# Kernel optimization log

Measured on AMD Instinct MI355X. Metric: run time of the kernel, lower is better.

## Reference

```python
import jax, jax.numpy as jnp
import numpy as np

T, B, D, H, A = 512, 1024, 128, 64, 18


def _mlp(x, W1, b1, W2, b2):
    # two Linear+ReLU layers (MLP with hidden_sizes=(64,64), output_dim=0)
    h = jax.nn.relu(x @ W1.T + b1)
    return jax.nn.relu(h @ W2.T + b2)


def _gru_scan(x, dones, h0, Wih, Whh, bih, bhh):
    # x: [T,B,H], dones: [T,B], h0: [1,B,H]; torch GRU cell with done-reset
    def step(h, inp):
        xt, dt = inp
        h = (1.0 - dt)[:, None] * h  # reset state where episode ended
        gi = xt @ Wih.T + bih        # [B,3H]
        gh = h @ Whh.T + bhh
        ir, iz, i_n = jnp.split(gi, 3, axis=-1)
        hr, hz, h_n = jnp.split(gh, 3, axis=-1)
        r = jax.nn.sigmoid(ir + hr)
        z = jax.nn.sigmoid(iz + hz)
        n = jnp.tanh(i_n + r * h_n)
        h_new = (1.0 - z) * n + z * h
        return h_new, h_new
    hT, hs = jax.lax.scan(step, h0[0], (x, dones))
    return hs, hT[None]  # [T,B,H], [1,B,H]


def setup_inputs() -> dict:
    key = jax.random.key(0)
    ks = jax.random.split(key, 24)
    u = lambda k, shape, fan_in: jax.random.uniform(k, shape, jnp.float32, -1.0, 1.0) / np.sqrt(fan_in)
    inp = {
        'obs': jax.random.normal(ks[0], (T, B, D), jnp.float32),
        'dones': (jax.random.uniform(ks[1], (T, B)) < 0.01).astype(jnp.float32),
        'actor_state': jnp.zeros((1, B, H), jnp.float32),
        'critic_state': jnp.zeros((1, B, H), jnp.float32),
        # actor params
        'aW1': u(ks[2], (H, D), D), 'ab1': u(ks[3], (H,), D),
        'aW2': u(ks[4], (H, H), H), 'ab2': u(ks[5], (H,), H),
        'aWih': u(ks[6], (3 * H, H), H), 'aWhh': u(ks[7], (3 * H, H), H),
        'abih': u(ks[8], (3 * H,), H), 'abhh': u(ks[9], (3 * H,), H),
        'aWl': u(ks[10], (A, H), H), 'abl': u(ks[11], (A,), H),
        # critic params
        'cW1': u(ks[12], (H, D), D), 'cb1': u(ks[13], (H,), D),
        'cW2': u(ks[14], (H, H), H), 'cb2': u(ks[15], (H,), H),
        'cWih': u(ks[16], (3 * H, H), H), 'cWhh': u(ks[17], (3 * H, H), H),
        'cbih': u(ks[18], (3 * H,), H), 'cbhh': u(ks[19], (3 * H,), H),
        'cWv': u(ks[20], (1, H), H), 'cbv': u(ks[21], (1,), H),
    }
    return inp


def reference(obs, dones, actor_state, critic_state,
              aW1, ab1, aW2, ab2, aWih, aWhh, abih, abhh, aWl, abl,
              cW1, cb1, cW2, cb2, cWih, cWhh, cbih, cbhh, cWv, cbv):
    # actor branch
    xa = _mlp(obs, aW1, ab1, aW2, ab2)                              # [T,B,H]
    ha, actor_state = _gru_scan(xa, dones, actor_state, aWih, aWhh, abih, abhh)
    logits = ha @ aWl.T + abl                                       # [T,B,A]
    # critic branch
    xc = _mlp(obs, cW1, cb1, cW2, cb2)
    hc, critic_state = _gru_scan(xc, dones, critic_state, cWih, cWhh, cbih, cbhh)
    values = hc @ cWv.T + cbv                                       # [T,B,1]
    return (logits, values, actor_state, critic_state)
```

## Files before the change

### kernel.cpp

```cpp
#include <hip/hip_runtime.h>
#include <hip/hip_bf16.h>

typedef short short8 __attribute__((ext_vector_type(8)));
typedef float f32x4 __attribute__((ext_vector_type(4)));

#define T_ 512
#define B_ 1024
#define D_ 128
#define H_ 64
#define A_ 18
#define TB_ (T_*B_)

#define XELEMS (TB_*H_)
#define WBASE  (2*XELEMS)
#define WBR    38912
#define W1OFF  0
#define W2OFF  8192
#define WIHOFF 12288
#define WHHOFF 24576
#define WHDOFF 36864

#define LOGN  (TB_*A_)
#define VOFF_ LOGN
#define SOFF_ (LOGN + TB_)

#define S1_ (-1.4426950408889634f)
#define S2_ (-2.885390081777927f)

__device__ __forceinline__ ushort f2bf(float f) {
  __hip_bfloat16 h = __float2bfloat16(f);
  return __builtin_bit_cast(ushort, h);
}
__device__ __forceinline__ uint cvt_pk_bf16(float lo, float hi) {
  uint r;
  asm("v_cvt_pk_bf16_f32 %0, %1, %2" : "=v"(r) : "v"(lo), "v"(hi));
  return r;
}
__device__ __forceinline__ ushort cvt1_bf16(float v) {
  return (ushort)(cvt_pk_bf16(v, v) & 0xffffu);
}
__device__ __forceinline__ f32x4 mfma16(short8 a, short8 b, f32x4 c) {
  return __builtin_amdgcn_mfma_f32_16x16x32_bf16(a, b, c, 0, 0, 0);
}

__global__ __launch_bounds__(256) void prep_kernel(
    const float* aW1, const float* aW2, const float* aWih, const float* aWhh, const float* aWl,
    const float* cW1, const float* cW2, const float* cWih, const float* cWhh, const float* cWv,
    ushort* wts) {
  int idx = blockIdx.x * 256 + threadIdx.x;
  if (idx >= 2*WBR) return;
  int br = idx / WBR, off = idx % WBR;
  float v;
  if      (off < W2OFF)  v = (br ? cW1  : aW1 )[off];
  else if (off < WIHOFF) v = (br ? cW2  : aW2 )[off - W2OFF];
  else if (off < WHHOFF) {
    int rel = off - WIHOFF;
    v = (br ? cWih : aWih)[rel];
    v *= (rel < 128*H_) ? S1_ : S2_;
  }
  else if (off < WHDOFF) {
    int rel = off - WHHOFF;
    v = (br ? cWhh : aWhh)[rel];
    v *= (rel < 128*H_) ? S1_ : S2_;
  }
  else {
    int t = off - WHDOFF;
    if (br == 0) v = (t < A_*H_) ? aWl[t] : 0.f;
    else         v = (t < H_)    ? cWv[t] : 0.f;
  }
  wts[WBASE + idx] = f2bf(v);
}

__global__ __launch_bounds__(256) void mlp_kernel(
    const float* __restrict__ obs, const ushort* __restrict__ wts,
    const float* __restrict__ ab1, const float* __restrict__ ab2,
    const float* __restrict__ cb1, const float* __restrict__ cb2,
    ushort* __restrict__ xout) {
  __shared__ __align__(16) ushort htA[4][16 * H_], htC[4][16 * H_];
  __shared__ __align__(16) ushort wlds[24576];
  const int tid = threadIdx.x;
  const int l = tid & 63, w = tid >> 6;
  const int lr = l & 15, lg = l >> 4;
  const int key = lr & 7;
  const long base = (long)blockIdx.x * 256;
  const ushort* wbA = wts + WBASE;
  const ushort* wbC = wts + WBASE + WBR;

  const int colq[2] = {lr, 16 + lr};
  float b1A[4], b1C[4], b2A[4], b2C[4];
  #pragma unroll
  for (int nt = 0; nt < 4; ++nt) {
    int coln = nt * 16 + lr;
    b1A[nt] = ab1[coln]; b1C[nt] = cb1[coln];
    b2A[nt] = ab2[coln]; b2C[nt] = cb2[coln];
  }
  (void)colq;

  #pragma unroll
  for (int i = 0; i < 12; ++i) {
    int c = tid + i * 256;
    int seg = (c < 1024) ? 0 : (c < 2048) ? 1 : (c < 2560) ? 2 : 3;
    int cbase = (seg == 0) ? 0 : (seg == 1) ? 1024 : (seg == 2) ? 2048 : 2560;
    int off = (c - cbase) * 8;
    int L = (seg < 2) ? 128 : 64;
    int segdst = (seg == 0) ? 0 : (seg == 1) ? 8192 : (seg == 2) ? 16384 : 20480;
    const ushort* src = (seg == 0) ? wbA + W1OFF + off :
                        (seg == 1) ? wbC + W1OFF + off :
                        (seg == 2) ? wbA + W2OFF + off : wbC + W2OFF + off;
    int n = off / L, ci = (off % L) / 8;
    int cis = (ci & ~7) | ((ci & 7) ^ (n & 7));
    *(uint4*)(wlds + segdst + n * L + cis * 8) = *(const uint4*)src;
  }
  __syncthreads();

  auto getW1 = [&](int br, int n, int ks) -> short8 {
    int ci = ks * 4 + lg;
    int cis = (ci & 8) | ((ci & 7) ^ (n & 7));
    return *(const short8*)(wlds + br * 8192 + n * D_ + cis * 8);
  };
  auto getW2 = [&](int br, int n, int ks) -> short8 {
    int ci = ks * 4 + lg;
    int cis = ci ^ (n & 7);
    return *(const short8*)(wlds + 16384 + br * 4096 + n * H_ + cis * 8);
  };

  auto ldobs = [&](int s, float4 (&buf)[8]) {
    const float* op = obs + (base + s * 64 + (long)w * 16 + lr) * D_;
    #pragma unroll
    for (int ks = 0; ks < 4; ++ks) {
      buf[2 * ks]     = *(const float4*)(op + ks * 32 + lg * 8);
      buf[2 * ks + 1] = *(const float4*)(op + ks * 32 + lg * 8 + 4);
    }
  };

  auto compute = [&](int s, float4 (&buf)[8]) {
    short8 af[4];
    #pragma unroll
    for (int ks = 0; ks < 4; ++ks) {
      uint4 u;
      u.x = cvt_pk_bf16(buf[2 * ks].x, buf[2 * ks].y);
      u.y = cvt_pk_bf16(buf[2 * ks].z, buf[2 * ks].w);
      u.z = cvt_pk_bf16(buf[2 * ks + 1].x, buf[2 * ks + 1].y);
      u.w = cvt_pk_bf16(buf[2 * ks + 1].z, buf[2 * ks + 1].w);
      af[ks] = __builtin_bit_cast(short8, u);
    }
    f32x4 aA[4], aC[4];
    #pragma unroll
    for (int nt = 0; nt < 4; ++nt) {
      aA[nt] = f32x4{b1A[nt], b1A[nt], b1A[nt], b1A[nt]};
      aC[nt] = f32x4{b1C[nt], b1C[nt], b1C[nt], b1C[nt]};
    }
    #pragma unroll
    for (int ks = 0; ks < 4; ++ks) {
      #pragma unroll
      for (int nt = 0; nt < 4; ++nt) {
        int n = nt * 16 + lr;
        aA[nt] = mfma16(af[ks], getW1(0, n, ks), aA[nt]);
        aC[nt] = mfma16(af[ks], getW1(1, n, ks), aC[nt]);
      }
    }
    #pragma unroll
    for (int nt = 0; nt < 4; ++nt) {
      int coln = nt * 16 + lr;
      #pragma unroll
      for (int j = 0; j < 4; ++j) {
        int rw = lg * 4 + j;
        int idx = rw * H_ + ((((coln >> 3) ^ (rw & 7))) << 3) + (coln & 7);
        htA[w][idx] = cvt1_bf16(fmaxf(aA[nt][j], 0.f));
        htC[w][idx] = cvt1_bf16(fmaxf(aC[nt][j], 0.f));
      }
    }
    short8 a2A[2], a2C[2];
    #pragma unroll
    for (int ks = 0; ks < 2; ++ks) {
      int c = ks * 4 + lg;
      a2A[ks] = *(const short8*)(&htA[w][lr * H_ + ((c ^ key) << 3)]);
      a2C[ks] = *(const short8*)(&htC[w][lr * H_ + ((c ^ key) << 3)]);
    }
    f32x4 cA[4], cC[4];
    #pragma unroll
    for (int nt = 0; nt < 4; ++nt) {
      cA[nt] = f32x4{b2A[nt], b2A[nt], b2A[nt], b2A[nt]};
      cC[nt] = f32x4{b2C[nt], b2C[nt], b2C[nt], b2C[nt]};
    }
    #pragma unroll
    for (int ks = 0; ks < 2; ++ks) {
      #pragma unroll
      for (int nt = 0; nt < 4; ++nt) {
        int n = nt * 16 + lr;
        cA[nt] = mfma16(a2A[ks], getW2(0, n, ks), cA[nt]);
        cC[nt] = mfma16(a2C[ks], getW2(1, n, ks), cC[nt]);
      }
    }
    #pragma unroll
    for (int nt = 0; nt < 4; ++nt) {
      int coln = nt * 16 + lr;
      #pragma unroll
      for (int j = 0; j < 4; ++j) {
        int rw = lg * 4 + j;
        int idx = rw * H_ + ((((coln >> 3) ^ (rw & 7))) << 3) + (coln & 7);
        htA[w][idx] = cvt1_bf16(fmaxf(cA[nt][j], 0.f));
        htC[w][idx] = cvt1_bf16(fmaxf(cC[nt][j], 0.f));
      }
    }
    {
      long rt = base + s * 64 + (long)w * 16;
      ushort* dpA = xout + (size_t)rt * H_;
      ushort* dpC = xout + (size_t)XELEMS + (size_t)rt * H_;
      #pragma unroll
      for (int i = 0; i < 2; ++i) {
        int id = l + i * 64;
        int rr = id >> 3, cc = id & 7;
        uint4 vA = *(const uint4*)(&htA[w][rr * H_ + ((cc ^ (rr & 7)) << 3)]);
        *(uint4*)(dpA + rr * H_ + (cc << 3)) = vA;
        uint4 vC = *(const uint4*)(&htC[w][rr * H_ + ((cc ^ (rr & 7)) << 3)]);
        *(uint4*)(dpC + rr * H_ + (cc << 3)) = vC;
      }
    }
  };

  float4 bufA[8], bufB[8];
  ldobs(0, bufA);
  ldobs(1, bufB);
  compute(0, bufA);
  ldobs(2, bufA);
  compute(1, bufB);
  ldobs(3, bufB);
  compute(2, bufA);
  compute(3, bufB);
}

__global__ __launch_bounds__(256, 1) void scan_kernel(
    const ushort* __restrict__ wts,
    const ushort* __restrict__ xin,
    ushort* __restrict__ hist,
    const float* __restrict__ dones,
    const float* __restrict__ astate, const float* __restrict__ cstate,
    const float* __restrict__ abih, const float* __restrict__ abhh,
    const float* __restrict__ cbih, const float* __restrict__ cbhh,
    float* __restrict__ out) {
  __shared__ __align__(16) ushort hbuf[2][16 * H_];
  __shared__ __align__(8)  ushort dl16[T_ * 16];
  const int tid = threadIdx.x;
  const int l = tid & 63, w = tid >> 6;
  const int lr = l & 15, lg = l >> 4;
  const int grp = blockIdx.x & 1;
  const int b0 = (blockIdx.x >> 1) * 16;

  const ushort* wb = wts + grp * WBR;
  const ushort* xp = xin + (size_t)grp * XELEMS;
  ushort* hp = hist + (size_t)grp * XELEMS;
  const float* bihp = grp ? cbih : abih;
  const float* bhhp = grp ? cbhh : abhh;
  const float* st   = grp ? cstate : astate;

  #pragma unroll
  for (int i = 0; i < 8; ++i) {
    int s = tid + i * 256;
    int t = s >> 2, p = s & 3;
    float4 v = *(const float4*)(dones + (size_t)t * B_ + b0 + p * 4);
    uint lo = (v.x != 0.f ? 1u : 0u) | ((v.y != 0.f ? 1u : 0u) << 16);
    uint hi = (v.z != 0.f ? 1u : 0u) | ((v.w != 0.f ? 1u : 0u) << 16);
    *(uint2*)(&dl16[t * 16 + p * 4]) = uint2{lo, hi};
  }

  short8 ihW[3][2], hhW[3][2];
  #pragma unroll
  for (int g = 0; g < 3; ++g) {
    int n = g * 64 + w * 16 + lr;
    #pragma unroll
    for (int ks = 0; ks < 2; ++ks) {
      ihW[g][ks] = *(const short8*)(wb + WIHOFF + n * H_ + ks * 32 + lg * 8);
      hhW[g][ks] = *(const short8*)(wb + WHHOFF + n * H_ + ks * 32 + lg * 8);
    }
  }

  const int o4 = w * 16 + lg * 4;
  f32x4 bs0, bs1, binv, bhnv;
  {
    float4 a0 = *(const float4*)(bihp + o4),       h0v = *(const float4*)(bhhp + o4);
    float4 a1 = *(const float4*)(bihp + 64 + o4),  h1v = *(const float4*)(bhhp + 64 + o4);
    float4 a2 = *(const float4*)(bihp + 128 + o4), h2v = *(const float4*)(bhhp + 128 + o4);
    bs0[0]=S1_*(a0.x+h0v.x); bs0[1]=S1_*(a0.y+h0v.y); bs0[2]=S1_*(a0.z+h0v.z); bs0[3]=S1_*(a0.w+h0v.w);
    bs1[0]=S1_*(a1.x+h1v.x); bs1[1]=S1_*(a1.y+h1v.y); bs1[2]=S1_*(a1.z+h1v.z); bs1[3]=S1_*(a1.w+h1v.w);
    binv[0]=S2_*a2.x; binv[1]=S2_*a2.y; binv[2]=S2_*a2.z; binv[3]=S2_*a2.w;
    bhnv[0]=S2_*h2v.x; bhnv[1]=S2_*h2v.y; bhnv[2]=S2_*h2v.z; bhnv[3]=S2_*h2v.w;
  }

  const int myW = lr * H_ + (((w * 2 + (lg >> 1)) ^ (lr & 7)) << 3) + (lg & 1) * 4;
  const int rdA = lr * H_ + (((0 + lg) ^ (lr & 7)) << 3);
  const int rdB = lr * H_ + (((4 + lg) ^ (lr & 7)) << 3);

  float h_old[4];
  {
    float4 h0v = *(const float4*)(st + (size_t)(b0 + lr) * H_ + o4);
    bool rs0 = (dones[b0 + lr] != 0.f);
    h_old[0] = rs0 ? 0.f : h0v.x; h_old[1] = rs0 ? 0.f : h0v.y;
    h_old[2] = rs0 ? 0.f : h0v.z; h_old[3] = rs0 ? 0.f : h0v.w;
    uint2 hv;
    hv.x = cvt_pk_bf16(h_old[0], h_old[1]);
    hv.y = cvt_pk_bf16(h_old[2], h_old[3]);
    *(uint2*)(&hbuf[0][myW]) = hv;
  }

  __syncthreads();

  auto loadx = [&](int t, short8 (&f)[2]) {
    const ushort* p = xp + ((size_t)t * B_ + b0 + lr) * H_;
    f[0] = *(const short8*)(p + lg * 8);
    f[1] = *(const short8*)(p + 32 + lg * 8);
  };

  short8 buf0[2], buf1[2], buf2[2], buf3[2];
  loadx(0, buf0); loadx(1, buf1); loadx(2, buf2); loadx(3, buf3);

  f32x4 preA[3], preB[3];
  auto cpre = [&](short8 (&xb)[2], f32x4 (&pre)[3]) {
    pre[0] = bs0;  pre[1] = bs1;  pre[2] = binv;
    pre[0] = mfma16(ihW[0][0], xb[0], pre[0]); pre[0] = mfma16(ihW[0][1], xb[1], pre[0]);
    pre[1] = mfma16(ihW[1][0], xb[0], pre[1]); pre[1] = mfma16(ihW[1][1], xb[1], pre[1]);
    pre[2] = mfma16(ihW[2][0], xb[0], pre[2]); pre[2] = mfma16(ihW[2][1], xb[1], pre[2]);
  };
  cpre(buf0, preA);

  int cur = 0;

  auto dostep = [&](int t, short8 (&xcur)[2], short8 (&xnext)[2],
                    f32x4 (&preU)[3], f32x4 (&preN)[3]) {
    short8 hf0 = *(const short8*)(&hbuf[cur][rdA]);
    short8 hf1 = *(const short8*)(&hbuf[cur][rdB]);
    int tn = t + 1;
    ushort dn = dl16[((tn < T_) ? tn : 0) * 16 + lr];
    bool rs = (tn < T_) && (dn != 0);

    f32x4 S0 = preU[0], S1 = preU[1], Gh = bhnv;
    S0 = mfma16(hhW[0][0], hf0, S0); S0 = mfma16(hhW[0][1], hf1, S0);
    S1 = mfma16(hhW[1][0], hf0, S1); S1 = mfma16(hhW[1][1], hf1, S1);
    Gh = mfma16(hhW[2][0], hf0, Gh); Gh = mfma16(hhW[2][1], hf1, Gh);

    cpre(xnext, preN);
    int tp = (t + 4 < T_) ? t + 4 : T_ - 1;
    loadx(tp, xcur);

    float hn[4];
    #pragma unroll
    for (int j = 0; j < 4; ++j) {
      float rr = __builtin_amdgcn_rcpf(1.f + __builtin_amdgcn_exp2f(S0[j]));
      float zz = __builtin_amdgcn_rcpf(1.f + __builtin_amdgcn_exp2f(S1[j]));
      float sn = fmaf(rr, Gh[j], preU[2][j]);
      float qq = __builtin_amdgcn_rcpf(1.f + __builtin_amdgcn_exp2f(sn));
      float nn = fmaf(2.f, qq, -1.f);
      hn[j] = fmaf(zz, h_old[j] - nn, nn);
    }
    uint2 hv;
    hv.x = cvt_pk_bf16(hn[0], hn[1]);
    hv.y = cvt_pk_bf16(hn[2], hn[3]);
    *(uint2*)(hp + ((size_t)t * B_ + b0 + lr) * H_ + o4) = hv;
    uint2 hz;
    hz.x = rs ? 0u : hv.x;
    hz.y = rs ? 0u : hv.y;
    h_old[0] = rs ? 0.f : hn[0]; h_old[1] = rs ? 0.f : hn[1];
    h_old[2] = rs ? 0.f : hn[2]; h_old[3] = rs ? 0.f : hn[3];
    int nxt = cur ^ 1;
    *(uint2*)(&hbuf[nxt][myW]) = hz;
    asm volatile("s_waitcnt lgkmcnt(0)" ::: "memory");
    __builtin_amdgcn_s_barrier();
    cur = nxt;
  };

  for (int it = 0; it < T_ / 4; ++it) {
    dostep(4 * it,     buf0, buf1, preA, preB);
    dostep(4 * it + 1, buf1, buf2, preB, preA);
    dostep(4 * it + 2, buf2, buf3, preA, preB);
    dostep(4 * it + 3, buf3, buf0, preB, preA);
  }

  float4 fs = {h_old[0], h_old[1], h_old[2], h_old[3]};
  *(float4*)(out + SOFF_ + (size_t)grp * (B_ * H_) + (size_t)(b0 + lr) * H_ + o4) = fs;
}

__global__ __launch_bounds__(256) void head_kernel(
    const ushort* __restrict__ ws,
    const float* __restrict__ abl, const float* __restrict__ cbv,
    float* __restrict__ out) {
  __shared__ float ltile[4][16 * A_];
  const int tid = threadIdx.x;
  const int l = tid & 63, w = tid >> 6;
  const int lr = l & 15, lg = l >> 4;
  const long r0 = (long)blockIdx.x * 64 + w * 16;
  const f32x4 fzero = {0.f, 0.f, 0.f, 0.f};

  const ushort* hA = ws + r0 * H_;
  const ushort* hC = ws + XELEMS + r0 * H_;
  short8 aA[2], aC[2];
  #pragma unroll
  for (int ks = 0; ks < 2; ++ks) {
    aA[ks] = *(const short8*)(hA + lr * H_ + ks * 32 + lg * 8);
    aC[ks] = *(const short8*)(hC + lr * H_ + ks * 32 + lg * 8);
  }
  const ushort* wbA = ws + WBASE + WHDOFF;
  const ushort* wbC = ws + WBASE + WBR + WHDOFF;
  f32x4 acc[2];
  acc[0] = fzero; acc[1] = fzero;
  #pragma unroll
  for (int nt = 0; nt < 2; ++nt) {
    int n = nt * 16 + lr;
    #pragma unroll
    for (int ks = 0; ks < 2; ++ks) {
      short8 b = *(const short8*)(wbA + n * H_ + ks * 32 + lg * 8);
      acc[nt] = mfma16(aA[ks], b, acc[nt]);
    }
  }
  f32x4 vacc = fzero;
  {
    int n = lr;
    #pragma unroll
    for (int ks = 0; ks < 2; ++ks) {
      short8 b = *(const short8*)(wbC + n * H_ + ks * 32 + lg * 8);
      vacc = mfma16(aC[ks], b, vacc);
    }
  }
  #pragma unroll
  for (int nt = 0; nt < 2; ++nt) {
    int n = nt * 16 + lr;
    if (n < A_) {
      float bias = abl[n];
      #pragma unroll
      for (int j = 0; j < 4; ++j)
        ltile[w][(lg * 4 + j) * A_ + n] = acc[nt][j] + bias;
    }
  }
  asm volatile("s_waitcnt lgkmcnt(0)" ::: "memory");
  #pragma unroll
  for (int i = 0; i < 5; ++i) {
    int idx = l + i * 64;
    if (idx < 16 * A_)
      out[r0 * A_ + idx] = ltile[w][idx];
  }
  if (lr == 0) {
    float bias = cbv[0];
    #pragma unroll
    for (int j = 0; j < 4; ++j)
      out[VOFF_ + r0 + lg * 4 + j] = vacc[j] + bias;
  }
}

extern "C" void kernel_launch(void* const* d_in, const int* in_sizes, int n_in,
                              void* d_out, int out_size, void* d_ws, size_t ws_size,
                              hipStream_t stream) {
  const float* obs    = (const float*)d_in[0];
  const float* dones  = (const float*)d_in[1];
  const float* astate = (const float*)d_in[2];
  const float* cstate = (const float*)d_in[3];
  const float* aW1  = (const float*)d_in[4];
  const float* ab1  = (const float*)d_in[5];
  const float* aW2  = (const float*)d_in[6];
  const float* ab2  = (const float*)d_in[7];
  const float* aWih = (const float*)d_in[8];
  const float* aWhh = (const float*)d_in[9];
  const float* abih = (const float*)d_in[10];
  const float* abhh = (const float*)d_in[11];
  const float* aWl  = (const float*)d_in[12];
  const float* abl  = (const float*)d_in[13];
  const float* cW1  = (const float*)d_in[14];
  const float* cb1  = (const float*)d_in[15];
  const float* cW2  = (const float*)d_in[16];
  const float* cb2  = (const float*)d_in[17];
  const float* cWih = (const float*)d_in[18];
  const float* cWhh = (const float*)d_in[19];
  const float* cbih = (const float*)d_in[20];
  const float* cbhh = (const float*)d_in[21];
  const float* cWv  = (const float*)d_in[22];
  const float* cbv  = (const float*)d_in[23];
  ushort* ws = (ushort*)d_ws;
  float* out = (float*)d_out;

  const size_t need = ((size_t)2 * XELEMS + 2 * WBR) * 2;
  if (ws_size < need) {
    hipMemsetAsync(d_out, 0x7F, 16, stream);
    return;
  }

  hipLaunchKernelGGL(prep_kernel, dim3(304), dim3(256), 0, stream,
                     aW1, aW2, aWih, aWhh, aWl, cW1, cW2, cWih, cWhh, cWv, ws);
  hipLaunchKernelGGL(mlp_kernel, dim3(TB_ / 256), dim3(256), 0, stream,
                     obs, ws, ab1, ab2, cb1, cb2, ws);
  hipLaunchKernelGGL(scan_kernel, dim3(128), dim3(256), 0, stream,
                     ws + WBASE, ws, ws, dones, astate, cstate,
                     abih, abhh, cbih, cbhh, out);
  hipLaunchKernelGGL(head_kernel, dim3(TB_ / 64), dim3(256), 0, stream,
                     ws, abl, cbv, out);
}
```

Baseline: 343.0 us.

## Process actor and critic GRU scans together per block with 8-row batches

The scan kernel now has each block handle both the actor and critic GRUs for 8 batch rows, instead of one GRU for 16 rows. The grid grows from 128 to 128 blocks of 8 rows each, but every block does two independent recurrences. Their MFMA chains can interleave within a single barrier per step, hiding latency and halving the number of per-step barriers across the two scans. In exchange, half of the MFMA rows are duplicated padding (lanes 8-15 repeat rows 0-7), which wastes compute, and register pressure doubles.

Result: slower. 470.4 us (+37.1%).

```diff
diff --git a/kernel.cpp b/kernel.cpp
--- a/kernel.cpp
+++ b/kernel.cpp
@@ -86,7 +86,6 @@
   const ushort* wbA = wts + WBASE;
   const ushort* wbC = wts + WBASE + WBR;
 
-  const int colq[2] = {lr, 16 + lr};
   float b1A[4], b1C[4], b2A[4], b2C[4];
   #pragma unroll
   for (int nt = 0; nt < 4; ++nt) {
@@ -94,7 +93,6 @@
     b1A[nt] = ab1[coln]; b1C[nt] = cb1[coln];
     b2A[nt] = ab2[coln]; b2C[nt] = cb2[coln];
   }
-  (void)colq;
 
   #pragma unroll
   for (int i = 0; i < 12; ++i) {
@@ -239,144 +237,194 @@
     const float* __restrict__ abih, const float* __restrict__ abhh,
     const float* __restrict__ cbih, const float* __restrict__ cbhh,
     float* __restrict__ out) {
-  __shared__ __align__(16) ushort hbuf[2][16 * H_];
-  __shared__ __align__(8)  ushort dl16[T_ * 16];
+  __shared__ __align__(16) ushort hbufA[2][16 * H_];
+  __shared__ __align__(16) ushort hbufC[2][16 * H_];
+  __shared__ __align__(8)  ushort dl8[T_ * 8];
   const int tid = threadIdx.x;
   const int l = tid & 63, w = tid >> 6;
   const int lr = l & 15, lg = l >> 4;
-  const int grp = blockIdx.x & 1;
-  const int b0 = (blockIdx.x >> 1) * 16;
-
-  const ushort* wb = wts + grp * WBR;
-  const ushort* xp = xin + (size_t)grp * XELEMS;
-  ushort* hp = hist + (size_t)grp * XELEMS;
-  const float* bihp = grp ? cbih : abih;
-  const float* bhhp = grp ? cbhh : abhh;
-  const float* st   = grp ? cstate : astate;
-
-  #pragma unroll
-  for (int i = 0; i < 8; ++i) {
-    int s = tid + i * 256;
-    int t = s >> 2, p = s & 3;
-    float4 v = *(const float4*)(dones + (size_t)t * B_ + b0 + p * 4);
-    uint lo = (v.x != 0.f ? 1u : 0u) | ((v.y != 0.f ? 1u : 0u) << 16);
-    uint hi = (v.z != 0.f ? 1u : 0u) | ((v.w != 0.f ? 1u : 0u) << 16);
-    *(uint2*)(&dl16[t * 16 + p * 4]) = uint2{lo, hi};
-  }
-
-  short8 ihW[3][2], hhW[3][2];
+  const int lrb = lr & 7;
+  const int b0 = blockIdx.x * 8;
+
+  const ushort* wbA = wts;
+  const ushort* wbC = wts + WBR;
+  const ushort* xpA = xin;
+  const ushort* xpC = xin + (size_t)XELEMS;
+  ushort* hpA = hist;
+  ushort* hpC = hist + (size_t)XELEMS;
+
+  #pragma unroll
+  for (int i = 0; i < 16; ++i) {
+    int idx = tid + i * 256;
+    int t = idx >> 3, p = idx & 7;
+    dl8[idx] = (dones[(size_t)t * B_ + b0 + p] != 0.f) ? 1 : 0;
+    (void)t; (void)p;
+  }
+
+  short8 ihA[3][2], hhA[3][2], ihC[3][2], hhC[3][2];
   #pragma unroll
   for (int g = 0; g < 3; ++g) {
     int n = g * 64 + w * 16 + lr;
     #pragma unroll
     for (int ks = 0; ks < 2; ++ks) {
-      ihW[g][ks] = *(const short8*)(wb + WIHOFF + n * H_ + ks * 32 + lg * 8);
-      hhW[g][ks] = *(const short8*)(wb + WHHOFF + n * H_ + ks * 32 + lg * 8);
+      ihA[g][ks] = *(const short8*)(wbA + WIHOFF + n * H_ + ks * 32 + lg * 8);
+      hhA[g][ks] = *(const short8*)(wbA + WHHOFF + n * H_ + ks * 32 + lg * 8);
+      ihC[g][ks] = *(const short8*)(wbC + WIHOFF + n * H_ + ks * 32 + lg * 8);
+      hhC[g][ks] = *(const short8*)(wbC + WHHOFF + n * H_ + ks * 32 + lg * 8);
     }
   }
 
   const int o4 = w * 16 + lg * 4;
-  f32x4 bs0, bs1, binv, bhnv;
-  {
-    float4 a0 = *(const float4*)(bihp + o4),       h0v = *(const float4*)(bhhp + o4);
-    float4 a1 = *(const float4*)(bihp + 64 + o4),  h1v = *(const float4*)(bhhp + 64 + o4);
-    float4 a2 = *(const float4*)(bihp + 128 + o4), h2v = *(const float4*)(bhhp + 128 + o4);
-    bs0[0]=S1_*(a0.x+h0v.x); bs0[1]=S1_*(a0.y+h0v.y); bs0[2]=S1_*(a0.z+h0v.z); bs0[3]=S1_*(a0.w+h0v.w);
-    bs1[0]=S1_*(a1.x+h1v.x); bs1[1]=S1_*(a1.y+h1v.y); bs1[2]=S1_*(a1.z+h1v.z); bs1[3]=S1_*(a1.w+h1v.w);
-    binv[0]=S2_*a2.x; binv[1]=S2_*a2.y; binv[2]=S2_*a2.z; binv[3]=S2_*a2.w;
-    bhnv[0]=S2_*h2v.x; bhnv[1]=S2_*h2v.y; bhnv[2]=S2_*h2v.z; bhnv[3]=S2_*h2v.w;
+  f32x4 bsA0, bsA1, bnA, bhA, bsC0, bsC1, bnC, bhC;
+  #pragma unroll
+  for (int q = 0; q < 2; ++q) {
+    const float* bi = q ? cbih : abih;
+    const float* bh = q ? cbhh : abhh;
+    float4 a0 = *(const float4*)(bi + o4),       h0v = *(const float4*)(bh + o4);
+    float4 a1 = *(const float4*)(bi + 64 + o4),  h1v = *(const float4*)(bh + 64 + o4);
+    float4 a2 = *(const float4*)(bi + 128 + o4), h2v = *(const float4*)(bh + 128 + o4);
+    f32x4 s0, s1, nv, hv;
+    s0[0]=S1_*(a0.x+h0v.x); s0[1]=S1_*(a0.y+h0v.y); s0[2]=S1_*(a0.z+h0v.z); s0[3]=S1_*(a0.w+h0v.w);
+    s1[0]=S1_*(a1.x+h1v.x); s1[1]=S1_*(a1.y+h1v.y); s1[2]=S1_*(a1.z+h1v.z); s1[3]=S1_*(a1.w+h1v.w);
+    nv[0]=S2_*a2.x; nv[1]=S2_*a2.y; nv[2]=S2_*a2.z; nv[3]=S2_*a2.w;
+    hv[0]=S2_*h2v.x; hv[1]=S2_*h2v.y; hv[2]=S2_*h2v.z; hv[3]=S2_*h2v.w;
+    if (q) { bsC0=s0; bsC1=s1; bnC=nv; bhC=hv; } else { bsA0=s0; bsA1=s1; bnA=nv; bhA=hv; }
   }
 
   const int myW = lr * H_ + (((w * 2 + (lg >> 1)) ^ (lr & 7)) << 3) + (lg & 1) * 4;
   const int rdA = lr * H_ + (((0 + lg) ^ (lr & 7)) << 3);
   const int rdB = lr * H_ + (((4 + lg) ^ (lr & 7)) << 3);
 
-  float h_old[4];
+  float hA_old[4], hC_old[4];
   {
-    float4 h0v = *(const float4*)(st + (size_t)(b0 + lr) * H_ + o4);
-    bool rs0 = (dones[b0 + lr] != 0.f);
-    h_old[0] = rs0 ? 0.f : h0v.x; h_old[1] = rs0 ? 0.f : h0v.y;
-    h_old[2] = rs0 ? 0.f : h0v.z; h_old[3] = rs0 ? 0.f : h0v.w;
+    float4 ha = *(const float4*)(astate + (size_t)(b0 + lrb) * H_ + o4);
+    float4 hc = *(const float4*)(cstate + (size_t)(b0 + lrb) * H_ + o4);
+    bool rs0 = (dones[b0 + lrb] != 0.f);
+    hA_old[0] = rs0 ? 0.f : ha.x; hA_old[1] = rs0 ? 0.f : ha.y;
+    hA_old[2] = rs0 ? 0.f : ha.z; hA_old[3] = rs0 ? 0.f : ha.w;
+    hC_old[0] = rs0 ? 0.f : hc.x; hC_old[1] = rs0 ? 0.f : hc.y;
+    hC_old[2] = rs0 ? 0.f : hc.z; hC_old[3] = rs0 ? 0.f : hc.w;
     uint2 hv;
-    hv.x = cvt_pk_bf16(h_old[0], h_old[1]);
-    hv.y = cvt_pk_bf16(h_old[2], h_old[3]);
-    *(uint2*)(&hbuf[0][myW]) = hv;
+    hv.x = cvt_pk_bf16(hA_old[0], hA_old[1]);
+    hv.y = cvt_pk_bf16(hA_old[2], hA_old[3]);
+    *(uint2*)(&hbufA[0][myW]) = hv;
+    hv.x = cvt_pk_bf16(hC_old[0], hC_old[1]);
+    hv.y = cvt_pk_bf16(hC_old[2], hC_old[3]);
+    *(uint2*)(&hbufC[0][myW]) = hv;
   }
 
   __syncthreads();
 
-  auto loadx = [&](int t, short8 (&f)[2]) {
-    const ushort* p = xp + ((size_t)t * B_ + b0 + lr) * H_;
+  auto loadx = [&](const ushort* xp, int t, short8 (&f)[2]) {
+    const ushort* p = xp + ((size_t)t * B_ + b0 + lrb) * H_;
     f[0] = *(const short8*)(p + lg * 8);
     f[1] = *(const short8*)(p + 32 + lg * 8);
   };
 
-  short8 buf0[2], buf1[2], buf2[2], buf3[2];
-  loadx(0, buf0); loadx(1, buf1); loadx(2, buf2); loadx(3, buf3);
-
-  f32x4 preA[3], preB[3];
-  auto cpre = [&](short8 (&xb)[2], f32x4 (&pre)[3]) {
-    pre[0] = bs0;  pre[1] = bs1;  pre[2] = binv;
-    pre[0] = mfma16(ihW[0][0], xb[0], pre[0]); pre[0] = mfma16(ihW[0][1], xb[1], pre[0]);
-    pre[1] = mfma16(ihW[1][0], xb[0], pre[1]); pre[1] = mfma16(ihW[1][1], xb[1], pre[1]);
-    pre[2] = mfma16(ihW[2][0], xb[0], pre[2]); pre[2] = mfma16(ihW[2][1], xb[1], pre[2]);
-  };
-  cpre(buf0, preA);
+  short8 bA0[2], bA1[2], bA2[2], bA3[2], bC0[2], bC1[2], bC2[2], bC3[2];
+  loadx(xpA, 0, bA0); loadx(xpA, 1, bA1); loadx(xpA, 2, bA2); loadx(xpA, 3, bA3);
+  loadx(xpC, 0, bC0); loadx(xpC, 1, bC1); loadx(xpC, 2, bC2); loadx(xpC, 3, bC3);
+
+  f32x4 pAa[3], pAb[3], pCa[3], pCb[3];
+  auto cpreA = [&](short8 (&xb)[2], f32x4 (&pre)[3]) {
+    pre[0] = bsA0;  pre[1] = bsA1;  pre[2] = bnA;
+    pre[0] = mfma16(ihA[0][0], xb[0], pre[0]); pre[0] = mfma16(ihA[0][1], xb[1], pre[0]);
+    pre[1] = mfma16(ihA[1][0], xb[0], pre[1]); pre[1] = mfma16(ihA[1][1], xb[1], pre[1]);
+    pre[2] = mfma16(ihA[2][0], xb[0], pre[2]); pre[2] = mfma16(ihA[2][1], xb[1], pre[2]);
+  };
+  auto cpreC = [&](short8 (&xb)[2], f32x4 (&pre)[3]) {
+    pre[0] = bsC0;  pre[1] = bsC1;  pre[2] = bnC;
+    pre[0] = mfma16(ihC[0][0], xb[0], pre[0]); pre[0] = mfma16(ihC[0][1], xb[1], pre[0]);
+    pre[1] = mfma16(ihC[1][0], xb[0], pre[1]); pre[1] = mfma16(ihC[1][1], xb[1], pre[1]);
+    pre[2] = mfma16(ihC[2][0], xb[0], pre[2]); pre[2] = mfma16(ihC[2][1], xb[1], pre[2]);
+  };
+  cpreA(bA0, pAa);
+  cpreC(bC0, pCa);
 
   int cur = 0;
 
-  auto dostep = [&](int t, short8 (&xcur)[2], short8 (&xnext)[2],
-                    f32x4 (&preU)[3], f32x4 (&preN)[3]) {
-    short8 hf0 = *(const short8*)(&hbuf[cur][rdA]);
-    short8 hf1 = *(const short8*)(&hbuf[cur][rdB]);
+  auto dostep = [&](int t, short8 (&xcA)[2], short8 (&xnA)[2], f32x4 (&pUA)[3], f32x4 (&pNA)[3],
+                    short8 (&xcC)[2], short8 (&xnC)[2], f32x4 (&pUC)[3], f32x4 (&pNC)[3]) {
+    short8 hfA0 = *(const short8*)(&hbufA[cur][rdA]);
+    short8 hfA1 = *(const short8*)(&hbufA[cur][rdB]);
+    short8 hfC0 = *(const short8*)(&hbufC[cur][rdA]);
+    short8 hfC1 = *(const short8*)(&hbufC[cur][rdB]);
     int tn = t + 1;
-    ushort dn = dl16[((tn < T_) ? tn : 0) * 16 + lr];
+    ushort dn = dl8[((tn < T_) ? tn : 0) * 8 + lrb];
     bool rs = (tn < T_) && (dn != 0);
 
-    f32x4 S0 = preU[0], S1 = preU[1], Gh = bhnv;
-    S0 = mfma16(hhW[0][0], hf0, S0); S0 = mfma16(hhW[0][1], hf1, S0);
-    S1 = mfma16(hhW[1][0], hf0, S1); S1 = mfma16(hhW[1][1], hf1, S1);
-    Gh = mfma16(hhW[2][0], hf0, Gh); Gh = mfma16(hhW[2][1], hf1, Gh);
-
-    cpre(xnext, preN);
+    f32x4 SA0 = pUA[0], SA1 = pUA[1], GA = bhA;
+    f32x4 SC0 = pUC[0], SC1 = pUC[1], GC = bhC;
+    SA0 = mfma16(hhA[0][0], hfA0, SA0); SA0 = mfma16(hhA[0][1], hfA1, SA0);
+    SC0 = mfma16(hhC[0][0], hfC0, SC0); SC0 = mfma16(hhC[0][1], hfC1, SC0);
+    SA1 = mfma16(hhA[1][0], hfA0, SA1); SA1 = mfma16(hhA[1][1], hfA1, SA1);
+    SC1 = mfma16(hhC[1][0], hfC0, SC1); SC1 = mfma16(hhC[1][1], hfC1, SC1);
+    GA  = mfma16(hhA[2][0], hfA0, GA);  GA  = mfma16(hhA[2][1], hfA1, GA);
+    GC  = mfma16(hhC[2][0], hfC0, GC);  GC  = mfma16(hhC[2][1], hfC1, GC);
+
+    cpreA(xnA, pNA);
+    cpreC(xnC, pNC);
     int tp = (t + 4 < T_) ? t + 4 : T_ - 1;
-    loadx(tp, xcur);
-
-    float hn[4];
+    loadx(xpA, tp, xcA);
+    loadx(xpC, tp, xcC);
+
+    float hnA[4], hnC[4];
     #pragma unroll
     for (int j = 0; j < 4; ++j) {
-      float rr = __builtin_amdgcn_rcpf(1.f + __builtin_amdgcn_exp2f(S0[j]));
-      float zz = __builtin_amdgcn_rcpf(1.f + __builtin_amdgcn_exp2f(S1[j]));
-      float sn = fmaf(rr, Gh[j], preU[2][j]);
+      float rr = __builtin_amdgcn_rcpf(1.f + __builtin_amdgcn_exp2f(SA0[j]));
+      float zz = __builtin_amdgcn_rcpf(1.f + __builtin_amdgcn_exp2f(SA1[j]));
+      float sn = fmaf(rr, GA[j], pUA[2][j]);
       float qq = __builtin_amdgcn_rcpf(1.f + __builtin_amdgcn_exp2f(sn));
       float nn = fmaf(2.f, qq, -1.f);
-      hn[j] = fmaf(zz, h_old[j] - nn, nn);
-    }
-    uint2 hv;
-    hv.x = cvt_pk_bf16(hn[0], hn[1]);
-    hv.y = cvt_pk_bf16(hn[2], hn[3]);
-    *(uint2*)(hp + ((size_t)t * B_ + b0 + lr) * H_ + o4) = hv;
-    uint2 hz;
-    hz.x = rs ? 0u : hv.x;
-    hz.y = rs ? 0u : hv.y;
-    h_old[0] = rs ? 0.f : hn[0]; h_old[1] = rs ? 0.f : hn[1];
-    h_old[2] = rs ? 0.f : hn[2]; h_old[3] = rs ? 0.f : hn[3];
+      hnA[j] = fmaf(zz, hA_old[j] - nn, nn);
+    }
+    #pragma unroll
+    for (int j = 0; j < 4; ++j) {
+      float rr = __builtin_amdgcn_rcpf(1.f + __builtin_amdgcn_exp2f(SC0[j]));
+      float zz = __builtin_amdgcn_rcpf(1.f + __builtin_amdgcn_exp2f(SC1[j]));
+      float sn = fmaf(rr, GC[j], pUC[2][j]);
+      float qq = __builtin_amdgcn_rcpf(1.f + __builtin_amdgcn_exp2f(sn));
+      float nn = fmaf(2.f, qq, -1.f);
+      hnC[j] = fmaf(zz, hC_old[j] - nn, nn);
+    }
+    uint2 hvA, hvC;
+    hvA.x = cvt_pk_bf16(hnA[0], hnA[1]);
+    hvA.y = cvt_pk_bf16(hnA[2], hnA[3]);
+    hvC.x = cvt_pk_bf16(hnC[0], hnC[1]);
+    hvC.y = cvt_pk_bf16(hnC[2], hnC[3]);
+    if (lr < 8) {
+      *(uint2*)(hpA + ((size_t)t * B_ + b0 + lrb) * H_ + o4) = hvA;
+      *(uint2*)(hpC + ((size_t)t * B_ + b0 + lrb) * H_ + o4) = hvC;
+    }
+    uint2 hzA, hzC;
+    hzA.x = rs ? 0u : hvA.x;  hzA.y = rs ? 0u : hvA.y;
+    hzC.x = rs ? 0u : hvC.x;  hzC.y = rs ? 0u : hvC.y;
+    #pragma unroll
+    for (int j = 0; j < 4; ++j) {
+      hA_old[j] = rs ? 0.f : hnA[j];
+      hC_old[j] = rs ? 0.f : hnC[j];
+    }
     int nxt = cur ^ 1;
-    *(uint2*)(&hbuf[nxt][myW]) = hz;
+    *(uint2*)(&hbufA[nxt][myW]) = hzA;
+    *(uint2*)(&hbufC[nxt][myW]) = hzC;
     asm volatile("s_waitcnt lgkmcnt(0)" ::: "memory");
     __builtin_amdgcn_s_barrier();
     cur = nxt;
   };
 
   for (int it = 0; it < T_ / 4; ++it) {
-    dostep(4 * it,     buf0, buf1, preA, preB);
-    dostep(4 * it + 1, buf1, buf2, preB, preA);
-    dostep(4 * it + 2, buf2, buf3, preA, preB);
-    dostep(4 * it + 3, buf3, buf0, preB, preA);
-  }
-
-  float4 fs = {h_old[0], h_old[1], h_old[2], h_old[3]};
-  *(float4*)(out + SOFF_ + (size_t)grp * (B_ * H_) + (size_t)(b0 + lr) * H_ + o4) = fs;
+    dostep(4 * it,     bA0, bA1, pAa, pAb, bC0, bC1, pCa, pCb);
+    dostep(4 * it + 1, bA1, bA2, pAb, pAa, bC1, bC2, pCb, pCa);
+    dostep(4 * it + 2, bA2, bA3, pAa, pAb, bC2, bC3, pCa, pCb);
+    dostep(4 * it + 3, bA3, bA0, pAb, pAa, bC3, bC0, pCb, pCa);
+  }
+
+  if (lr < 8) {
+    float4 fa = {hA_old[0], hA_old[1], hA_old[2], hA_old[3]};
+    float4 fc = {hC_old[0], hC_old[1], hC_old[2], hC_old[3]};
+    *(float4*)(out + SOFF_ + (size_t)(b0 + lrb) * H_ + o4) = fa;
+    *(float4*)(out + SOFF_ + (size_t)B_ * H_ + (size_t)(b0 + lrb) * H_ + o4) = fc;
+  }
 }
 
 __global__ __launch_bounds__(256) void head_kernel(
@@ -485,7 +533,7 @@
                      aW1, aW2, aWih, aWhh, aWl, cW1, cW2, cWih, cWhh, cWv, ws);
   hipLaunchKernelGGL(mlp_kernel, dim3(TB_ / 256), dim3(256), 0, stream,
                      obs, ws, ab1, ab2, cb1, cb2, ws);
-  hipLaunchKernelGGL(scan_kernel, dim3(128), dim3(256), 0, stream,
+  hipLaunchKernelGGL(scan_kernel, dim3(B_ / 8), dim3(256), 0, stream,
                      ws + WBASE, ws, ws, dones, astate, cstate,
                      abih, abhh, cbih, cbhh, out);
   hipLaunchKernelGGL(head_kernel, dim3(TB_ / 64), dim3(256), 0, stream,
```

## Split scan block into recurrence and producer warps exchanging through LDS

Applied to the files above, without the earlier changes.

The GRU scan kernel now runs 512 threads per block. Four waves do only the recurrent h·Whh MFMAs and gate math. The other four waves compute the input projection for the next step, prefetch x, and write the previous step's hidden state to global memory. Data moves between the two sets of waves through double-buffered LDS arrays, so global loads, stores and the input MFMAs leave the serial critical path. The cost is extra LDS traffic per step and a barrier that now spans all eight waves.

New measurement: 329.4 us. 1.04x faster.

```diff
diff --git a/kernel.cpp b/kernel.cpp
--- a/kernel.cpp
+++ b/kernel.cpp
@@ -86,7 +86,6 @@
   const ushort* wbA = wts + WBASE;
   const ushort* wbC = wts + WBASE + WBR;
 
-  const int colq[2] = {lr, 16 + lr};
   float b1A[4], b1C[4], b2A[4], b2C[4];
   #pragma unroll
   for (int nt = 0; nt < 4; ++nt) {
@@ -94,7 +93,6 @@
     b1A[nt] = ab1[coln]; b1C[nt] = cb1[coln];
     b2A[nt] = ab2[coln]; b2C[nt] = cb2[coln];
   }
-  (void)colq;
 
   #pragma unroll
   for (int i = 0; i < 12; ++i) {
@@ -230,7 +228,7 @@
   compute(3, bufB);
 }
 
-__global__ __launch_bounds__(256, 1) void scan_kernel(
+__global__ __launch_bounds__(512, 1) void scan_kernel(
     const ushort* __restrict__ wts,
     const ushort* __restrict__ xin,
     ushort* __restrict__ hist,
@@ -241,11 +239,16 @@
     float* __restrict__ out) {
   __shared__ __align__(16) ushort hbuf[2][16 * H_];
   __shared__ __align__(8)  ushort dl16[T_ * 16];
+  __shared__ __align__(16) float  preL[2][3][1024];
+  __shared__ __align__(8)  uint2  hhist[2][256];
   const int tid = threadIdx.x;
   const int l = tid & 63, w = tid >> 6;
+  const int pw = w & 3;
   const int lr = l & 15, lg = l >> 4;
   const int grp = blockIdx.x & 1;
   const int b0 = (blockIdx.x >> 1) * 16;
+  const int slot = pw * 64 + ((l & ~7) | ((l ^ (l >> 3)) & 7));
+  const int o4 = pw * 16 + lg * 4;
 
   const ushort* wb = wts + grp * WBR;
   const ushort* xp = xin + (size_t)grp * XELEMS;
@@ -255,8 +258,8 @@
   const float* st   = grp ? cstate : astate;
 
   #pragma unroll
-  for (int i = 0; i < 8; ++i) {
-    int s = tid + i * 256;
+  for (int i = 0; i < 4; ++i) {
+    int s = tid + i * 512;
     int t = s >> 2, p = s & 3;
     float4 v = *(const float4*)(dones + (size_t)t * B_ + b0 + p * 4);
     uint lo = (v.x != 0.f ? 1u : 0u) | ((v.y != 0.f ? 1u : 0u) << 16);
@@ -264,35 +267,43 @@
     *(uint2*)(&dl16[t * 16 + p * 4]) = uint2{lo, hi};
   }
 
-  short8 ihW[3][2], hhW[3][2];
-  #pragma unroll
-  for (int g = 0; g < 3; ++g) {
-    int n = g * 64 + w * 16 + lr;
-    #pragma unroll
-    for (int ks = 0; ks < 2; ++ks) {
-      ihW[g][ks] = *(const short8*)(wb + WIHOFF + n * H_ + ks * 32 + lg * 8);
-      hhW[g][ks] = *(const short8*)(wb + WHHOFF + n * H_ + ks * 32 + lg * 8);
-    }
-  }
-
-  const int o4 = w * 16 + lg * 4;
-  f32x4 bs0, bs1, binv, bhnv;
-  {
-    float4 a0 = *(const float4*)(bihp + o4),       h0v = *(const float4*)(bhhp + o4);
-    float4 a1 = *(const float4*)(bihp + 64 + o4),  h1v = *(const float4*)(bhhp + 64 + o4);
-    float4 a2 = *(const float4*)(bihp + 128 + o4), h2v = *(const float4*)(bhhp + 128 + o4);
-    bs0[0]=S1_*(a0.x+h0v.x); bs0[1]=S1_*(a0.y+h0v.y); bs0[2]=S1_*(a0.z+h0v.z); bs0[3]=S1_*(a0.w+h0v.w);
-    bs1[0]=S1_*(a1.x+h1v.x); bs1[1]=S1_*(a1.y+h1v.y); bs1[2]=S1_*(a1.z+h1v.z); bs1[3]=S1_*(a1.w+h1v.w);
-    binv[0]=S2_*a2.x; binv[1]=S2_*a2.y; binv[2]=S2_*a2.z; binv[3]=S2_*a2.w;
-    bhnv[0]=S2_*h2v.x; bhnv[1]=S2_*h2v.y; bhnv[2]=S2_*h2v.z; bhnv[3]=S2_*h2v.w;
-  }
-
-  const int myW = lr * H_ + (((w * 2 + (lg >> 1)) ^ (lr & 7)) << 3) + (lg & 1) * 4;
+  short8 hhW[3][2];
+  f32x4 bhnv;
+  float h_old[4];
+  const int myW = lr * H_ + (((pw * 2 + (lg >> 1)) ^ (lr & 7)) << 3) + (lg & 1) * 4;
   const int rdA = lr * H_ + (((0 + lg) ^ (lr & 7)) << 3);
   const int rdB = lr * H_ + (((4 + lg) ^ (lr & 7)) << 3);
 
-  float h_old[4];
-  {
+  short8 ihW[3][2];
+  f32x4 bs0, bs1, binv;
+  short8 pb0[2], pb1[2], pb2[2], pb3[2];
+
+  auto loadx = [&](int t, short8 (&f)[2]) {
+    const ushort* p = xp + ((size_t)t * B_ + b0 + lr) * H_;
+    f[0] = *(const short8*)(p + lg * 8);
+    f[1] = *(const short8*)(p + 32 + lg * 8);
+  };
+  auto cpre_to = [&](short8 (&xb)[2], int par) {
+    f32x4 p0 = bs0, p1 = bs1, p2 = binv;
+    p0 = mfma16(ihW[0][0], xb[0], p0); p0 = mfma16(ihW[0][1], xb[1], p0);
+    p1 = mfma16(ihW[1][0], xb[0], p1); p1 = mfma16(ihW[1][1], xb[1], p1);
+    p2 = mfma16(ihW[2][0], xb[0], p2); p2 = mfma16(ihW[2][1], xb[1], p2);
+    *(f32x4*)&preL[par][0][slot * 4] = p0;
+    *(f32x4*)&preL[par][1][slot * 4] = p1;
+    *(f32x4*)&preL[par][2][slot * 4] = p2;
+  };
+
+  if (w < 4) {
+    #pragma unroll
+    for (int g = 0; g < 3; ++g) {
+      int n = g * 64 + pw * 16 + lr;
+      #pragma unroll
+      for (int ks = 0; ks < 2; ++ks)
+        hhW[g][ks] = *(const short8*)(wb + WHHOFF + n * H_ + ks * 32 + lg * 8);
+    }
+    float4 h2v = *(const float4*)(bhhp + 128 + o4);
+    bhnv[0] = S2_ * h2v.x; bhnv[1] = S2_ * h2v.y;
+    bhnv[2] = S2_ * h2v.z; bhnv[3] = S2_ * h2v.w;
     float4 h0v = *(const float4*)(st + (size_t)(b0 + lr) * H_ + o4);
     bool rs0 = (dones[b0 + lr] != 0.f);
     h_old[0] = rs0 ? 0.f : h0v.x; h_old[1] = rs0 ? 0.f : h0v.y;
@@ -301,82 +312,94 @@
     hv.x = cvt_pk_bf16(h_old[0], h_old[1]);
     hv.y = cvt_pk_bf16(h_old[2], h_old[3]);
     *(uint2*)(&hbuf[0][myW]) = hv;
+  } else {
+    #pragma unroll
+    for (int g = 0; g < 3; ++g) {
+      int n = g * 64 + pw * 16 + lr;
+      #pragma unroll
+      for (int ks = 0; ks < 2; ++ks)
+        ihW[g][ks] = *(const short8*)(wb + WIHOFF + n * H_ + ks * 32 + lg * 8);
+    }
+    float4 a0 = *(const float4*)(bihp + o4),       h0v = *(const float4*)(bhhp + o4);
+    float4 a1 = *(const float4*)(bihp + 64 + o4),  h1v = *(const float4*)(bhhp + 64 + o4);
+    float4 a2 = *(const float4*)(bihp + 128 + o4);
+    bs0[0]=S1_*(a0.x+h0v.x); bs0[1]=S1_*(a0.y+h0v.y); bs0[2]=S1_*(a0.z+h0v.z); bs0[3]=S1_*(a0.w+h0v.w);
+    bs1[0]=S1_*(a1.x+h1v.x); bs1[1]=S1_*(a1.y+h1v.y); bs1[2]=S1_*(a1.z+h1v.z); bs1[3]=S1_*(a1.w+h1v.w);
+    binv[0]=S2_*a2.x; binv[1]=S2_*a2.y; binv[2]=S2_*a2.z; binv[3]=S2_*a2.w;
+    loadx(0, pb0);
+    cpre_to(pb0, 0);
+    loadx(1, pb1); loadx(2, pb2); loadx(3, pb3); loadx(4, pb0);
   }
 
   __syncthreads();
 
-  auto loadx = [&](int t, short8 (&f)[2]) {
-    const ushort* p = xp + ((size_t)t * B_ + b0 + lr) * H_;
-    f[0] = *(const short8*)(p + lg * 8);
-    f[1] = *(const short8*)(p + 32 + lg * 8);
-  };
-
-  short8 buf0[2], buf1[2], buf2[2], buf3[2];
-  loadx(0, buf0); loadx(1, buf1); loadx(2, buf2); loadx(3, buf3);
-
-  f32x4 preA[3], preB[3];
-  auto cpre = [&](short8 (&xb)[2], f32x4 (&pre)[3]) {
-    pre[0] = bs0;  pre[1] = bs1;  pre[2] = binv;
-    pre[0] = mfma16(ihW[0][0], xb[0], pre[0]); pre[0] = mfma16(ihW[0][1], xb[1], pre[0]);
-    pre[1] = mfma16(ihW[1][0], xb[0], pre[1]); pre[1] = mfma16(ihW[1][1], xb[1], pre[1]);
-    pre[2] = mfma16(ihW[2][0], xb[0], pre[2]); pre[2] = mfma16(ihW[2][1], xb[1], pre[2]);
-  };
-  cpre(buf0, preA);
-
-  int cur = 0;
-
-  auto dostep = [&](int t, short8 (&xcur)[2], short8 (&xnext)[2],
-                    f32x4 (&preU)[3], f32x4 (&preN)[3]) {
-    short8 hf0 = *(const short8*)(&hbuf[cur][rdA]);
-    short8 hf1 = *(const short8*)(&hbuf[cur][rdB]);
-    int tn = t + 1;
-    ushort dn = dl16[((tn < T_) ? tn : 0) * 16 + lr];
-    bool rs = (tn < T_) && (dn != 0);
-
-    f32x4 S0 = preU[0], S1 = preU[1], Gh = bhnv;
-    S0 = mfma16(hhW[0][0], hf0, S0); S0 = mfma16(hhW[0][1], hf1, S0);
-    S1 = mfma16(hhW[1][0], hf0, S1); S1 = mfma16(hhW[1][1], hf1, S1);
-    Gh = mfma16(hhW[2][0], hf0, Gh); Gh = mfma16(hhW[2][1], hf1, Gh);
-
-    cpre(xnext, preN);
-    int tp = (t + 4 < T_) ? t + 4 : T_ - 1;
-    loadx(tp, xcur);
-
-    float hn[4];
-    #pragma unroll
-    for (int j = 0; j < 4; ++j) {
-      float rr = __builtin_amdgcn_rcpf(1.f + __builtin_amdgcn_exp2f(S0[j]));
-      float zz = __builtin_amdgcn_rcpf(1.f + __builtin_amdgcn_exp2f(S1[j]));
-      float sn = fmaf(rr, Gh[j], preU[2][j]);
-      float qq = __builtin_amdgcn_rcpf(1.f + __builtin_amdgcn_exp2f(sn));
-      float nn = fmaf(2.f, qq, -1.f);
-      hn[j] = fmaf(zz, h_old[j] - nn, nn);
-    }
-    uint2 hv;
-    hv.x = cvt_pk_bf16(hn[0], hn[1]);
-    hv.y = cvt_pk_bf16(hn[2], hn[3]);
-    *(uint2*)(hp + ((size_t)t * B_ + b0 + lr) * H_ + o4) = hv;
-    uint2 hz;
-    hz.x = rs ? 0u : hv.x;
-    hz.y = rs ? 0u : hv.y;
-    h_old[0] = rs ? 0.f : hn[0]; h_old[1] = rs ? 0.f : hn[1];
-    h_old[2] = rs ? 0.f : hn[2]; h_old[3] = rs ? 0.f : hn[3];
-    int nxt = cur ^ 1;
-    *(uint2*)(&hbuf[nxt][myW]) = hz;
-    asm volatile("s_waitcnt lgkmcnt(0)" ::: "memory");
-    __builtin_amdgcn_s_barrier();
-    cur = nxt;
-  };
-
-  for (int it = 0; it < T_ / 4; ++it) {
-    dostep(4 * it,     buf0, buf1, preA, preB);
-    dostep(4 * it + 1, buf1, buf2, preB, preA);
-    dostep(4 * it + 2, buf2, buf3, preA, preB);
-    dostep(4 * it + 3, buf3, buf0, preB, preA);
-  }
-
-  float4 fs = {h_old[0], h_old[1], h_old[2], h_old[3]};
-  *(float4*)(out + SOFF_ + (size_t)grp * (B_ * H_) + (size_t)(b0 + lr) * H_ + o4) = fs;
+  if (w < 4) {
+    int cur = 0;
+    auto cstep = [&](int t) {
+      short8 hf0 = *(const short8*)(&hbuf[cur][rdA]);
+      short8 hf1 = *(const short8*)(&hbuf[cur][rdB]);
+      int par = t & 1;
+      f32x4 S0 = *(const f32x4*)&preL[par][0][slot * 4];
+      f32x4 S1 = *(const f32x4*)&preL[par][1][slot * 4];
+      f32x4 P2 = *(const f32x4*)&preL[par][2][slot * 4];
+      f32x4 Gh = bhnv;
+      int tn = t + 1;
+      ushort dn = dl16[((tn < T_) ? tn : 0) * 16 + lr];
+      bool rs = (tn < T_) && (dn != 0);
+
+      S0 = mfma16(hhW[0][0], hf0, S0); S0 = mfma16(hhW[0][1], hf1, S0);
+      S1 = mfma16(hhW[1][0], hf0, S1); S1 = mfma16(hhW[1][1], hf1, S1);
+      Gh = mfma16(hhW[2][0], hf0, Gh); Gh = mfma16(hhW[2][1], hf1, Gh);
+
+      float hn[4];
+      #pragma unroll
+      for (int j = 0; j < 4; ++j) {
+        float rr = __builtin_amdgcn_rcpf(1.f + __builtin_amdgcn_exp2f(S0[j]));
+        float zz = __builtin_amdgcn_rcpf(1.f + __builtin_amdgcn_exp2f(S1[j]));
+        float sn = fmaf(rr, Gh[j], P2[j]);
+        float qq = __builtin_amdgcn_rcpf(1.f + __builtin_amdgcn_exp2f(sn));
+        float nn = fmaf(2.f, qq, -1.f);
+        hn[j] = fmaf(zz, h_old[j] - nn, nn);
+      }
+      uint2 hv;
+      hv.x = cvt_pk_bf16(hn[0], hn[1]);
+      hv.y = cvt_pk_bf16(hn[2], hn[3]);
+      hhist[par][slot] = hv;
+      uint2 hz;
+      hz.x = rs ? 0u : hv.x;
+      hz.y = rs ? 0u : hv.y;
+      h_old[0] = rs ? 0.f : hn[0]; h_old[1] = rs ? 0.f : hn[1];
+      h_old[2] = rs ? 0.f : hn[2]; h_old[3] = rs ? 0.f : hn[3];
+      int nxt = cur ^ 1;
+      *(uint2*)(&hbuf[nxt][myW]) = hz;
+      asm volatile("s_waitcnt lgkmcnt(0)" ::: "memory");
+      __builtin_amdgcn_s_barrier();
+      cur = nxt;
+    };
+    for (int t = 0; t < T_; ++t) cstep(t);
+    float4 fs = {h_old[0], h_old[1], h_old[2], h_old[3]};
+    *(float4*)(out + SOFF_ + (size_t)grp * (B_ * H_) + (size_t)(b0 + lr) * H_ + o4) = fs;
+  } else {
+    auto pstep = [&](int t, short8 (&xb)[2]) {
+      if (t > 0) {
+        uint2 hv2 = hhist[(t - 1) & 1][slot];
+        *(uint2*)(hp + ((size_t)(t - 1) * B_ + b0 + lr) * H_ + o4) = hv2;
+      }
+      if (t + 1 < T_) cpre_to(xb, (t + 1) & 1);
+      if (t + 5 < T_) loadx(t + 5, xb);
+      asm volatile("s_waitcnt lgkmcnt(0)" ::: "memory");
+      __builtin_amdgcn_s_barrier();
+    };
+    for (int it = 0; it < T_ / 4; ++it) {
+      int t = 4 * it;
+      pstep(t,     pb1);
+      pstep(t + 1, pb2);
+      pstep(t + 2, pb3);
+      pstep(t + 3, pb0);
+    }
+    uint2 hv2 = hhist[(T_ - 1) & 1][slot];
+    *(uint2*)(hp + ((size_t)(T_ - 1) * B_ + b0 + lr) * H_ + o4) = hv2;
+  }
 }
 
 __global__ __launch_bounds__(256) void head_kernel(
@@ -485,7 +508,7 @@
                      aW1, aW2, aWih, aWhh, aWl, cW1, cW2, cWih, cWhh, cWv, ws);
   hipLaunchKernelGGL(mlp_kernel, dim3(TB_ / 256), dim3(256), 0, stream,
                      obs, ws, ab1, ab2, cb1, cb2, ws);
-  hipLaunchKernelGGL(scan_kernel, dim3(128), dim3(256), 0, stream,
+  hipLaunchKernelGGL(scan_kernel, dim3(128), dim3(512), 0, stream,
                      ws + WBASE, ws, ws, dones, astate, cstate,
                      abih, abhh, cbih, cbhh, out);
   hipLaunchKernelGGL(head_kernel, dim3(TB_ / 64), dim3(256), 0, stream,
```
